# Optimization experiments

Hardware: AMD Instinct MI355X
Metric: run time of the kernel (lower is better)

The kernel has to match this reference:

```python
import jax, jax.numpy as jnp
import numpy as np
import math

B, T, D = 2, 2048, 2048
H = 16
HD = D // H
FF = D * 2


def rmsnorm(x, w):
    eps = jnp.finfo(x.dtype).eps  # torch RMSNorm default eps=None -> finfo eps
    ms = jnp.mean(jnp.square(x), axis=-1, keepdims=True)
    return x * jax.lax.rsqrt(ms + eps) * w


def setup_inputs() -> dict:
    key = jax.random.key(0)
    ks = jax.random.split(key, 8)
    s = 0.02
    return {
        "x": jax.random.normal(ks[0], (B, T, D), jnp.float32),
        "scale_gamma": jax.random.uniform(ks[1], (D,), jnp.float32, 0.5, 1.5),
        "scale_beta": jax.random.normal(ks[2], (D,), jnp.float32) * 0.1,
        "qkv_w": jax.random.normal(ks[3], (3 * D, D), jnp.float32) * s,
        "o_w": jax.random.normal(ks[4], (D, D), jnp.float32) * s,
        "gate_w": jax.random.normal(ks[5], (FF, D), jnp.float32) * s,
        "up_w": jax.random.normal(ks[6], (FF, D), jnp.float32) * s,
        "down_w": jax.random.normal(ks[7], (D, FF), jnp.float32) * s,
        "norm1_w": jnp.ones((D,), jnp.float32),
        "norm2_w": jnp.ones((D,), jnp.float32),
    }


def reference(x, scale_gamma, scale_beta, qkv_w, o_w, gate_w, up_w, down_w, norm1_w, norm2_w):
    # --- attention sub-block ---
    h = rmsnorm(x, norm1_w) * scale_gamma + scale_beta
    qkv = (h @ qkv_w.T).reshape(B, T, 3, H, HD)
    q, k, v = [jnp.transpose(qkv[:, :, i], (0, 2, 1, 3)) for i in range(3)]  # (B,H,T,HD)
    scores = jnp.einsum("bhqd,bhkd->bhqk", q, k) / math.sqrt(HD)
    causal = jnp.tril(jnp.ones((T, T), bool))
    scores = jnp.where(causal, scores, -jnp.inf)
    attn = jax.nn.softmax(scores, axis=-1)
    out = jnp.einsum("bhqk,bhkd->bhqd", attn, v)
    out = jnp.transpose(out, (0, 2, 1, 3)).reshape(B, T, D)
    x = x + out @ o_w.T
    # --- SwiGLU FFN sub-block ---
    h = rmsnorm(x, norm2_w) * scale_gamma + scale_beta
    ff = jax.nn.silu(h @ gate_w.T) * (h @ up_w.T)
    return x + ff @ down_w.T
```

## Files before the change

### kernel.cpp

```cpp
#include <hip/hip_runtime.h>
#include <cstdint>

#define D_MODEL 2048
#define T_SEQ   2048
#define BATCH   2
#define NHEAD   16
#define HDIM    128
#define FFDIM   4096
#define NTOK    4096

using bf16_t = __bf16;
typedef __attribute__((ext_vector_type(8))) __bf16 bf16x8;
typedef __attribute__((ext_vector_type(4))) __bf16 bf16x4;
typedef __attribute__((ext_vector_type(4))) float  f32x4;

typedef __attribute__((address_space(1))) void as1_void;
typedef __attribute__((address_space(3))) void as3_void;

__device__ __forceinline__ void async_copy16(const void* g, void* lds) {
  __builtin_amdgcn_global_load_lds((as1_void*)(uintptr_t)g,
                                   (as3_void*)(uint32_t)(uintptr_t)lds,
                                   16, 0, 0);
}

__device__ __forceinline__ size_t packidx(int n, int kc, int nkt) {
  int kt = kc >> 2, kg = kc & 3;
  return (((size_t)(n >> 7) * nkt + kt) << 9) + (kg << 7) + (n & 127);
}

#define NQ 1572864
#define NO 524288
#define NG 1048576
#define NU 1048576
#define ND 1048576
#define TOTC (NQ + NO + NG + NU + ND)
__global__ __launch_bounds__(256) void f2b_all_kernel(
    const float* __restrict__ s0, const float* __restrict__ s1,
    const float* __restrict__ s2, const float* __restrict__ s3,
    const float* __restrict__ s4,
    bf16_t* __restrict__ d0, bf16_t* __restrict__ d1,
    bf16_t* __restrict__ dgu, bf16_t* __restrict__ d4) {
  int c = blockIdx.x * 256 + threadIdx.x;
  const int stride = gridDim.x * 256;
  for (; c < TOTC; c += stride) {
    const float* src; bf16_t* dst; size_t didx; int sf4;
    if (c < NQ) {
      int n = c >> 8, kc = c & 255;
      src = s0; sf4 = n * 512 + kc * 2;
      dst = d0; didx = packidx(n, kc, 64);
    } else if (c < NQ + NO) {
      int lc = c - NQ, n = lc >> 8, kc = lc & 255;
      src = s1; sf4 = n * 512 + kc * 2;
      dst = d1; didx = packidx(n, kc, 64);
    } else if (c < NQ + NO + NG) {
      int lc = c - NQ - NO, g = lc >> 8, kc = lc & 255;
      int n2 = ((g >> 4) << 5) + (g & 15);
      src = s2; sf4 = g * 512 + kc * 2;
      dst = dgu; didx = packidx(n2, kc, 64);
    } else if (c < NQ + NO + NG + NU) {
      int lc = c - NQ - NO - NG, u = lc >> 8, kc = lc & 255;
      int n2 = ((u >> 4) << 5) + 16 + (u & 15);
      src = s3; sf4 = u * 512 + kc * 2;
      dst = dgu; didx = packidx(n2, kc, 64);
    } else {
      int lc = c - NQ - NO - NG - NU, n = lc >> 9, kc = lc & 511;
      src = s4; sf4 = n * 1024 + kc * 2;
      dst = d4; didx = packidx(n, kc, 128);
    }
    float4 v0 = ((const float4*)src)[sf4];
    float4 v1 = ((const float4*)src)[sf4 + 1];
    bf16x8 r;
    r[0] = (bf16_t)v0.x; r[1] = (bf16_t)v0.y; r[2] = (bf16_t)v0.z; r[3] = (bf16_t)v0.w;
    r[4] = (bf16_t)v1.x; r[5] = (bf16_t)v1.y; r[6] = (bf16_t)v1.z; r[7] = (bf16_t)v1.w;
    *(bf16x8*)(dst + didx * 8) = r;
  }
}

__global__ __launch_bounds__(256) void rmsnorm_kernel(const float* __restrict__ x,
                                                      const float* __restrict__ nw,
                                                      const float* __restrict__ gamma,
                                                      const float* __restrict__ beta,
                                                      bf16_t* __restrict__ out) {
  const int row = blockIdx.x;
  const int t = threadIdx.x;
  const float* xr = x + (size_t)row * D_MODEL;
  float4 va = ((const float4*)xr)[2 * t];
  float4 vb = ((const float4*)xr)[2 * t + 1];
  float ss = va.x*va.x + va.y*va.y + va.z*va.z + va.w*va.w
           + vb.x*vb.x + vb.y*vb.y + vb.z*vb.z + vb.w*vb.w;
#pragma unroll
  for (int off = 1; off < 64; off <<= 1) ss += __shfl_xor(ss, off, 64);
  __shared__ float sred[4];
  if ((t & 63) == 0) sred[t >> 6] = ss;
  __syncthreads();
  float tot = sred[0] + sred[1] + sred[2] + sred[3];
  float inv = rsqrtf(tot * (1.0f / D_MODEL) + 1.1920929e-07f);
  const int c0 = t * 8;
  float a8[8] = {va.x, va.y, va.z, va.w, vb.x, vb.y, vb.z, vb.w};
  bf16x8 r;
#pragma unroll
  for (int j = 0; j < 8; ++j)
    r[j] = (bf16_t)(a8[j] * inv * nw[c0 + j] * gamma[c0 + j] + beta[c0 + j]);
  *(bf16x8*)(out + packidx(row, t, 64) * 8) = r;
}

template <int EPI>
__global__ __launch_bounds__(256) void gemm_kernel(const bf16_t* __restrict__ A,
                                                   const bf16_t* __restrict__ Bw,
                                                   int M, int N, int K,
                                                   void* out, const void* aux) {
  __shared__ alignas(16) bf16_t As[2][4][128][8];
  __shared__ alignas(16) bf16_t Bs[2][4][128][8];
  const int tid = threadIdx.x;
  const int wave = tid >> 6, lane = tid & 63;
  const int quad = lane >> 4, l16 = lane & 15;
  const int bx = blockIdx.x, by = blockIdx.y;
  const int wr = (wave >> 1) * 64, wc = (wave & 1) * 64;
  const int rowA0 = by * 128, colB0 = bx * 128;

  const f32x4 fzero = {0.f, 0.f, 0.f, 0.f};
  f32x4 acc[4][4];
#pragma unroll
  for (int i = 0; i < 4; ++i)
#pragma unroll
    for (int j = 0; j < 4; ++j) acc[i][j] = fzero;

  const int nk = K >> 5;
  const bf16_t* a0 = A + ((size_t)by * nk << 12) + tid * 8;
  const bf16_t* a1 = a0 + 2048;
  const bf16_t* b0 = Bw + ((size_t)bx * nk << 12) + tid * 8;
  const bf16_t* b1 = b0 + 2048;
  char* ldsA0 = (char*)As + (wave * 64) * 16;
  char* ldsA1 = (char*)As + (256 + wave * 64) * 16;
  char* ldsB0 = (char*)Bs + (wave * 64) * 16;
  char* ldsB1 = (char*)Bs + (256 + wave * 64) * 16;

  async_copy16(a0, ldsA0);
  async_copy16(a1, ldsA1);
  async_copy16(b0, ldsB0);
  async_copy16(b1, ldsB1);
  a0 += 4096; a1 += 4096; b0 += 4096; b1 += 4096;

  for (int kt = 0; kt < nk; ++kt) {
    __syncthreads();
    const int cur = kt & 1;
    if (kt + 1 < nk) {
      const int nxt = 8192 * (1 - cur);
      async_copy16(a0, ldsA0 + nxt);
      async_copy16(a1, ldsA1 + nxt);
      async_copy16(b0, ldsB0 + nxt);
      async_copy16(b1, ldsB1 + nxt);
      a0 += 4096; a1 += 4096; b0 += 4096; b1 += 4096;
    }
    bf16x8 af[4], bfr[4];
#pragma unroll
    for (int mi = 0; mi < 4; ++mi)
      af[mi] = *(const bf16x8*)&As[cur][quad][wr + mi * 16 + l16][0];
#pragma unroll
    for (int ni = 0; ni < 4; ++ni)
      bfr[ni] = *(const bf16x8*)&Bs[cur][quad][wc + ni * 16 + l16][0];
#pragma unroll
    for (int mi = 0; mi < 4; ++mi)
#pragma unroll
      for (int ni = 0; ni < 4; ++ni)
        acc[mi][ni] = __builtin_amdgcn_mfma_f32_16x16x32_bf16(af[mi], bfr[ni],
                                                              acc[mi][ni], 0, 0, 0);
  }

  if (EPI == 4) {
#pragma unroll
    for (int mi = 0; mi < 4; ++mi) {
#pragma unroll
      for (int r = 0; r < 4; ++r) {
        const int row = rowA0 + wr + mi * 16 + quad * 4 + r;
        const int rt = row >> 7, m = row & 127;
#pragma unroll
        for (int p = 0; p < 2; ++p) {
          float g = acc[mi][2 * p][r];
          float u = acc[mi][2 * p + 1][r];
          float sv = g / (1.0f + __expf(-g));
          const int ffcol = bx * 64 + (wc >> 1) + l16 + p * 16;
          const int kt2 = ffcol >> 5, kg2 = (ffcol >> 3) & 3, e = ffcol & 7;
          const size_t idx =
              (((((size_t)rt * 128 + kt2) << 9) + (kg2 << 7) + m) << 3) + e;
          ((bf16_t*)out)[idx] = (bf16_t)(sv * u);
        }
      }
    }
  } else {
#pragma unroll
    for (int mi = 0; mi < 4; ++mi) {
#pragma unroll
      for (int r = 0; r < 4; ++r) {
        const int row = rowA0 + wr + mi * 16 + quad * 4 + r;
        const size_t base = (size_t)row * N;
#pragma unroll
        for (int ni = 0; ni < 4; ++ni) {
          const int col = colB0 + wc + ni * 16 + l16;
          const size_t idx = base + col;
          float v = acc[mi][ni][r];
          if (EPI == 0) {
            ((bf16_t*)out)[idx] = (bf16_t)v;
          } else {
            ((float*)out)[idx] = v + ((const float*)aux)[idx];
          }
        }
      }
    }
  }
}

__global__ __launch_bounds__(256) void vtrans_kernel(const bf16_t* __restrict__ qkv,
                                                     bf16_t* __restrict__ vt) {
  const int bh = blockIdx.y;
  const int b = bh >> 4, h = bh & 15;
  const int t0 = blockIdx.x << 6;
  const int tid = threadIdx.x;
  __shared__ bf16_t tile[64][136];
#pragma unroll
  for (int r = 0; r < 4; ++r) {
    int ci = r * 256 + tid;
    int t = ci >> 4, dc = ci & 15;
    bf16x8 v = *(const bf16x8*)(qkv + (size_t)(b * T_SEQ + t0 + t) * 6144 + 4096 +
                                h * HDIM + dc * 8);
    *(bf16x8*)&tile[t][dc * 8] = v;
  }
  __syncthreads();
#pragma unroll
  for (int r = 0; r < 4; ++r) {
    int ci = r * 256 + tid;
    int d = ci >> 3, ts = ci & 7;
    bf16x8 o;
#pragma unroll
    for (int j = 0; j < 8; ++j) o[j] = tile[ts * 8 + j][d];
    *(bf16x8*)(vt + ((size_t)bh * HDIM + d) * T_SEQ + t0 + ts * 8) = o;
  }
}

__global__ __launch_bounds__(256) void attn_kernel(const bf16_t* __restrict__ qkv,
                                                   const bf16_t* __restrict__ vt,
                                                   bf16_t* __restrict__ out) {
  const int bh = blockIdx.y;
  const int b = bh >> 4, h = bh & 15;
  const int qt = gridDim.x - 1 - blockIdx.x;
  const int q0 = qt << 6;
  const int tid = threadIdx.x;
  const int wave = tid >> 6, lane = tid & 63;
  const int quad = lane >> 4, l16 = lane & 15;

  __shared__ alignas(16) bf16_t Ks[2][64 * 128];
  __shared__ alignas(16) bf16_t VTs[2][128 * 64];
  __shared__ bf16_t Ps[4][16][68];

  const size_t qbase = (size_t)(b * T_SEQ + q0 + wave * 16 + l16) * 6144 + h * HDIM;
  bf16x8 qf[4];
#pragma unroll
  for (int kk = 0; kk < 4; ++kk)
    qf[kk] = *(const bf16x8*)(qkv + qbase + kk * 32 + quad * 8);

  const bf16_t* gK[4];
  const bf16_t* gV[4];
#pragma unroll
  for (int c = 0; c < 4; ++c) {
    int ci = c * 256 + tid;
    int t = ci >> 4, dcs = ci & 15;
    int dc = dcs ^ (t & 15);
    gK[c] = qkv + (size_t)(b * T_SEQ + t) * 6144 + 2048 + h * HDIM + dc * 8;
    int d = ci >> 3, tcs = ci & 7;
    int tc = tcs ^ (d & 7);
    gV[c] = vt + ((size_t)bh * HDIM + d) * T_SEQ + tc * 8;
  }
  char* ldsK = (char*)Ks + wave * 1024;
  char* ldsV = (char*)VTs + wave * 1024;

  auto stage = [&](int buf) {
#pragma unroll
    for (int c = 0; c < 4; ++c) {
      async_copy16(gK[c], ldsK + buf * 16384 + c * 4096);
      gK[c] += 64 * 6144;
    }
#pragma unroll
    for (int c = 0; c < 4; ++c) {
      async_copy16(gV[c], ldsV + buf * 16384 + c * 4096);
      gV[c] += 64;
    }
  };

  const f32x4 fzero = {0.f, 0.f, 0.f, 0.f};
  f32x4 o[8];
#pragma unroll
  for (int i = 0; i < 8; ++i) o[i] = fzero;
  float mrow[4]  = {-3.0e38f, -3.0e38f, -3.0e38f, -3.0e38f};
  float lpart[4] = {0.f, 0.f, 0.f, 0.f};

  const float sc = 0.08838834764831845f;
  const float THR = 8.0f;
  const int ktmax = qt;

  stage(0);

  for (int kt = 0; kt <= ktmax; ++kt) {
    const int cur = kt & 1;
    __syncthreads();
    if (kt < ktmax) stage(1 - cur);

    const bf16_t* Kc = &Ks[cur][0];
    const bf16_t* Vc = &VTs[cur][0];

    f32x4 s[4];
#pragma unroll
    for (int nt = 0; nt < 4; ++nt) {
      s[nt] = fzero;
#pragma unroll
      for (int kk = 0; kk < 4; ++kk) {
        int tK = nt * 16 + l16;
        int cK = kk * 4 + quad;
        bf16x8 kf = *(const bf16x8*)(Kc + (tK * 16 + (cK ^ l16)) * 8);
        s[nt] = __builtin_amdgcn_mfma_f32_16x16x32_bf16(qf[kk], kf, s[nt], 0, 0, 0);
      }
    }

    const int qr0 = q0 + wave * 16 + quad * 4;
    const bool diag = (kt == ktmax);
    float pmax[4];
#pragma unroll
    for (int r = 0; r < 4; ++r) {
      const int qr = qr0 + r;
      float mx = -3.0e38f;
#pragma unroll
      for (int nt = 0; nt < 4; ++nt) {
        float v = s[nt][r] * sc;
        if (diag) {
          int kc = kt * 64 + nt * 16 + l16;
          v = (kc <= qr) ? v : -3.0e38f;
        }
        s[nt][r] = v;
        mx = fmaxf(mx, v);
      }
      pmax[r] = mx;
    }
    bool ok = (pmax[0] <= mrow[0] + THR) & (pmax[1] <= mrow[1] + THR) &
              (pmax[2] <= mrow[2] + THR) & (pmax[3] <= mrow[3] + THR);
    if (!__all(ok)) {
      float alpha[4];
#pragma unroll
      for (int r = 0; r < 4; ++r) {
        float mx = pmax[r];
#pragma unroll
        for (int off = 1; off < 16; off <<= 1) mx = fmaxf(mx, __shfl_xor(mx, off, 16));
        float mnew = fmaxf(mrow[r], mx);
        alpha[r] = __expf(mrow[r] - mnew);
        mrow[r] = mnew;
        lpart[r] *= alpha[r];
      }
#pragma unroll
      for (int i = 0; i < 8; ++i)
#pragma unroll
        for (int r = 0; r < 4; ++r) o[i][r] *= alpha[r];
    }
#pragma unroll
    for (int r = 0; r < 4; ++r) {
#pragma unroll
      for (int nt = 0; nt < 4; ++nt) {
        float pv = __expf(s[nt][r] - mrow[r]);
        s[nt][r] = pv;
        lpart[r] += pv;
      }
    }
#pragma unroll
    for (int nt = 0; nt < 4; ++nt)
#pragma unroll
      for (int r = 0; r < 4; ++r)
        Ps[wave][quad * 4 + r][nt * 16 + l16] = (bf16_t)s[nt][r];

#pragma unroll
    for (int kk2 = 0; kk2 < 2; ++kk2) {
      const bf16_t* prow = &Ps[wave][l16][kk2 * 32 + quad * 8];
      bf16x4 p0 = *(const bf16x4*)prow;
      bf16x4 p1 = *(const bf16x4*)(prow + 4);
      bf16x8 pf;
#pragma unroll
      for (int j = 0; j < 4; ++j) { pf[j] = p0[j]; pf[4 + j] = p1[j]; }
#pragma unroll
      for (int nt2 = 0; nt2 < 8; ++nt2) {
        int dV = nt2 * 16 + l16;
        int tcV = kk2 * 4 + quad;
        bf16x8 vf = *(const bf16x8*)(Vc + (dV * 8 + (tcV ^ (dV & 7))) * 8);
        o[nt2] = __builtin_amdgcn_mfma_f32_16x16x32_bf16(pf, vf, o[nt2], 0, 0, 0);
      }
    }
  }

  float rl[4];
#pragma unroll
  for (int r = 0; r < 4; ++r) {
    float l = lpart[r];
#pragma unroll
    for (int off = 1; off < 16; off <<= 1) l += __shfl_xor(l, off, 16);
    rl[r] = 1.0f / l;
  }
#pragma unroll
  for (int nt2 = 0; nt2 < 8; ++nt2) {
#pragma unroll
    for (int r = 0; r < 4; ++r) {
      const int gt = b * T_SEQ + q0 + wave * 16 + quad * 4 + r;
      const int mt = gt >> 7, m = gt & 127;
      const int col = h * HDIM + nt2 * 16 + l16;
      const int kt2 = col >> 5, kg2 = (col >> 3) & 3, e = col & 7;
      const size_t idx = (((((size_t)mt * 64 + kt2) << 9) + (kg2 << 7) + m) << 3) + e;
      out[idx] = (bf16_t)(o[nt2][r] * rl[r]);
    }
  }
}

extern "C" void kernel_launch(void* const* d_in, const int* in_sizes, int n_in,
                              void* d_out, int out_size, void* d_ws, size_t ws_size,
                              hipStream_t stream) {
  const float* x      = (const float*)d_in[0];
  const float* gamma  = (const float*)d_in[1];
  const float* beta   = (const float*)d_in[2];
  const float* qkv_w  = (const float*)d_in[3];
  const float* o_w    = (const float*)d_in[4];
  const float* gate_w = (const float*)d_in[5];
  const float* up_w   = (const float*)d_in[6];
  const float* down_w = (const float*)d_in[7];
  const float* n1w    = (const float*)d_in[8];
  const float* n2w    = (const float*)d_in[9];
  float* out = (float*)d_out;

  char* p = (char*)d_ws;
  bf16_t* qkv_wb  = (bf16_t*)p; p += (size_t)3 * D_MODEL * D_MODEL * 2;
  bf16_t* o_wb    = (bf16_t*)p; p += (size_t)D_MODEL * D_MODEL * 2;
  bf16_t* gu_wb   = (bf16_t*)p; p += (size_t)2 * FFDIM * D_MODEL * 2;
  bf16_t* down_wb = (bf16_t*)p; p += (size_t)D_MODEL * FFDIM * 2;
  bf16_t* h_b     = (bf16_t*)p; p += (size_t)NTOK * D_MODEL * 2;
  bf16_t* qkv_b   = (bf16_t*)p; p += (size_t)NTOK * 3 * D_MODEL * 2;
  bf16_t* attn_b  = (bf16_t*)p; p += (size_t)NTOK * D_MODEL * 2;
  float*  x1      = (float*)p;  p += (size_t)NTOK * D_MODEL * 4;
  bf16_t* g_b     = (bf16_t*)p; p += (size_t)NTOK * FFDIM * 2;
  bf16_t* vt_b    = g_b;

  dim3 blk(256);
  f2b_all_kernel<<<dim3(2048), blk, 0, stream>>>(
      qkv_w, o_w, gate_w, up_w, down_w,
      qkv_wb, o_wb, gu_wb, down_wb);

  rmsnorm_kernel<<<dim3(NTOK), blk, 0, stream>>>(x, n1w, gamma, beta, h_b);
  gemm_kernel<0><<<dim3(3 * D_MODEL / 128, NTOK / 128), blk, 0, stream>>>(
      h_b, qkv_wb, NTOK, 3 * D_MODEL, D_MODEL, qkv_b, nullptr);
  vtrans_kernel<<<dim3(T_SEQ / 64, BATCH * NHEAD), blk, 0, stream>>>(qkv_b, vt_b);
  attn_kernel<<<dim3(T_SEQ / 64, BATCH * NHEAD), blk, 0, stream>>>(qkv_b, vt_b, attn_b);
  gemm_kernel<1><<<dim3(D_MODEL / 128, NTOK / 128), blk, 0, stream>>>(
      attn_b, o_wb, NTOK, D_MODEL, D_MODEL, x1, x);

  rmsnorm_kernel<<<dim3(NTOK), blk, 0, stream>>>(x1, n2w, gamma, beta, h_b);
  gemm_kernel<4><<<dim3(2 * FFDIM / 128, NTOK / 128), blk, 0, stream>>>(
      h_b, gu_wb, NTOK, 2 * FFDIM, D_MODEL, g_b, nullptr);
  gemm_kernel<1><<<dim3(D_MODEL / 128, NTOK / 128), blk, 0, stream>>>(
      g_b, down_wb, NTOK, D_MODEL, FFDIM, out, x1);
}
```

Baseline: 815.3 us.

## Add 256x256-tile GEMM with 4-stage async pipeline for QKV and gate/up

Introduces a 512-thread GEMM kernel with 256x256 output tiles, a 4-deep LDS ring of async global-to-LDS copies, interleaved load/MFMA phases with priority hints, and an XCD-aware block swizzle. It replaces the 128x128 GEMM for the QKV projection and the fused gate/up SwiGLU GEMM, aiming at more data reuse per tile and better overlap of loads with compute. The old kernel's SwiGLU epilogue is removed. Tradeoffs are 128KB of LDS, higher register pressure and fewer blocks on these grids.

```diff
diff --git a/kernel.cpp b/kernel.cpp
--- a/kernel.cpp
+++ b/kernel.cpp
@@ -21,6 +21,10 @@
   __builtin_amdgcn_global_load_lds((as1_void*)(uintptr_t)g,
                                    (as3_void*)(uint32_t)(uintptr_t)lds,
                                    16, 0, 0);
+}
+
+__device__ __forceinline__ void barrier_raw() {
+  asm volatile("s_barrier" ::: "memory");
 }
 
 __device__ __forceinline__ size_t packidx(int n, int kc, int nkt) {
@@ -105,6 +109,133 @@
 }
 
 template <int EPI>
+__global__ __launch_bounds__(512, 2) void gemm256_kernel(
+    const bf16_t* __restrict__ A, const bf16_t* __restrict__ Bw,
+    int M, int N, int K, void* out) {
+  __shared__ alignas(16) char ldsbuf[131072];
+  const int tid = threadIdx.x;
+  const int wave = tid >> 6, lane = tid & 63;
+  const int quad = lane >> 4, l16 = lane & 15;
+  const int wm = wave >> 2, wn = wave & 3;
+
+  const int gx = gridDim.x;
+  const int lin = blockIdx.y * gx + blockIdx.x;
+  const int cpx = (gx * gridDim.y) >> 3;
+  const int swz = (lin & 7) * cpx + (lin >> 3);
+  const int bx = swz % gx, by = swz / gx;
+
+  const int nk = K >> 5;
+  const char* pA0 = (const char*)A  + (((size_t)(2 * by)     * nk) << 13) + tid * 16;
+  const char* pA1 = (const char*)A  + (((size_t)(2 * by + 1) * nk) << 13) + tid * 16;
+  const char* pB0 = (const char*)Bw + (((size_t)(2 * bx)     * nk) << 13) + tid * 16;
+  const char* pB1 = (const char*)Bw + (((size_t)(2 * bx + 1) * nk) << 13) + tid * 16;
+
+  auto stageA = [&](int b) {
+    async_copy16(pA0, ldsbuf + (b << 15) + wave * 1024);
+    async_copy16(pA1, ldsbuf + (b << 15) + 8192 + wave * 1024);
+    pA0 += 8192; pA1 += 8192;
+  };
+  auto stageB = [&](int b) {
+    async_copy16(pB0, ldsbuf + (b << 15) + 16384 + wave * 1024);
+    async_copy16(pB1, ldsbuf + (b << 15) + 24576 + wave * 1024);
+    pB0 += 8192; pB1 += 8192;
+  };
+
+  const f32x4 fzero = {0.f, 0.f, 0.f, 0.f};
+  f32x4 acc[8][4];
+#pragma unroll
+  for (int i = 0; i < 8; ++i)
+#pragma unroll
+    for (int j = 0; j < 4; ++j) acc[i][j] = fzero;
+
+  stageA(0); stageB(0); stageA(1); stageB(1); stageA(2); stageB(2);
+  asm volatile("s_waitcnt vmcnt(8)" ::: "memory");
+  barrier_raw();
+
+  for (int j = 0; j < nk; ++j) {
+    const int b = j & 3;
+    const int bs = (b + 3) & 3;
+    const bool more = (j + 3 < nk);
+    const char* Ab = ldsbuf + (b << 15) + (wm << 13) + (quad << 11);
+    const char* Bb = ldsbuf + (b << 15) + 16384 + ((wn >> 1) << 13) + (quad << 11) +
+                     ((wn & 1) << 10);
+    bf16x8 af[4], bfr[4];
+#pragma unroll
+    for (int mi = 0; mi < 4; ++mi)
+      af[mi] = *(const bf16x8*)(Ab + (mi * 16 + l16) * 16);
+#pragma unroll
+    for (int ni = 0; ni < 4; ++ni)
+      bfr[ni] = *(const bf16x8*)(Bb + (ni * 16 + l16) * 16);
+    if (more) stageA(bs);
+    barrier_raw();
+    __builtin_amdgcn_s_setprio(1);
+#pragma unroll
+    for (int mi = 0; mi < 4; ++mi)
+#pragma unroll
+      for (int ni = 0; ni < 4; ++ni)
+        acc[mi][ni] = __builtin_amdgcn_mfma_f32_16x16x32_bf16(af[mi], bfr[ni],
+                                                              acc[mi][ni], 0, 0, 0);
+    __builtin_amdgcn_s_setprio(0);
+    barrier_raw();
+#pragma unroll
+    for (int mi = 0; mi < 4; ++mi)
+      af[mi] = *(const bf16x8*)(Ab + ((mi + 4) * 16 + l16) * 16);
+    if (more) stageB(bs);
+    barrier_raw();
+    __builtin_amdgcn_s_setprio(1);
+#pragma unroll
+    for (int mi = 0; mi < 4; ++mi)
+#pragma unroll
+      for (int ni = 0; ni < 4; ++ni)
+        acc[mi + 4][ni] = __builtin_amdgcn_mfma_f32_16x16x32_bf16(af[mi], bfr[ni],
+                                                                  acc[mi + 4][ni], 0, 0, 0);
+    __builtin_amdgcn_s_setprio(0);
+    if (j + 3 < nk)      asm volatile("s_waitcnt vmcnt(8)" ::: "memory");
+    else if (j + 2 < nk) asm volatile("s_waitcnt vmcnt(4)" ::: "memory");
+    else if (j + 1 < nk) asm volatile("s_waitcnt vmcnt(0)" ::: "memory");
+    barrier_raw();
+  }
+
+  const int rowbase = by * 256 + wm * 128;
+  const int colbase = bx * 256 + wn * 64;
+  if (EPI == 4) {
+#pragma unroll
+    for (int mi = 0; mi < 8; ++mi) {
+#pragma unroll
+      for (int r = 0; r < 4; ++r) {
+        const int row = rowbase + mi * 16 + quad * 4 + r;
+        const int rt = row >> 7, m = row & 127;
+#pragma unroll
+        for (int p = 0; p < 2; ++p) {
+          float g = acc[mi][2 * p][r];
+          float u = acc[mi][2 * p + 1][r];
+          float sv = g / (1.0f + __expf(-g));
+          const int ffcol = (bx * 8 + wn * 2 + p) * 16 + l16;
+          const int kt2 = ffcol >> 5, kg2 = (ffcol >> 3) & 3, e = ffcol & 7;
+          const size_t idx =
+              (((((size_t)rt * 128 + kt2) << 9) + (kg2 << 7) + m) << 3) + e;
+          ((bf16_t*)out)[idx] = (bf16_t)(sv * u);
+        }
+      }
+    }
+  } else {
+#pragma unroll
+    for (int mi = 0; mi < 8; ++mi) {
+#pragma unroll
+      for (int r = 0; r < 4; ++r) {
+        const int row = rowbase + mi * 16 + quad * 4 + r;
+        const size_t base = (size_t)row * N;
+#pragma unroll
+        for (int ni = 0; ni < 4; ++ni) {
+          const int col = colbase + ni * 16 + l16;
+          ((bf16_t*)out)[base + col] = (bf16_t)acc[mi][ni][r];
+        }
+      }
+    }
+  }
+}
+
+template <int EPI>
 __global__ __launch_bounds__(256) void gemm_kernel(const bf16_t* __restrict__ A,
                                                    const bf16_t* __restrict__ Bw,
                                                    int M, int N, int K,
@@ -167,43 +298,21 @@
                                                               acc[mi][ni], 0, 0, 0);
   }
 
-  if (EPI == 4) {
-#pragma unroll
-    for (int mi = 0; mi < 4; ++mi) {
-#pragma unroll
-      for (int r = 0; r < 4; ++r) {
-        const int row = rowA0 + wr + mi * 16 + quad * 4 + r;
-        const int rt = row >> 7, m = row & 127;
-#pragma unroll
-        for (int p = 0; p < 2; ++p) {
-          float g = acc[mi][2 * p][r];
-          float u = acc[mi][2 * p + 1][r];
-          float sv = g / (1.0f + __expf(-g));
-          const int ffcol = bx * 64 + (wc >> 1) + l16 + p * 16;
-          const int kt2 = ffcol >> 5, kg2 = (ffcol >> 3) & 3, e = ffcol & 7;
-          const size_t idx =
-              (((((size_t)rt * 128 + kt2) << 9) + (kg2 << 7) + m) << 3) + e;
-          ((bf16_t*)out)[idx] = (bf16_t)(sv * u);
-        }
-      }
-    }
-  } else {
-#pragma unroll
-    for (int mi = 0; mi < 4; ++mi) {
-#pragma unroll
-      for (int r = 0; r < 4; ++r) {
-        const int row = rowA0 + wr + mi * 16 + quad * 4 + r;
-        const size_t base = (size_t)row * N;
-#pragma unroll
-        for (int ni = 0; ni < 4; ++ni) {
-          const int col = colB0 + wc + ni * 16 + l16;
-          const size_t idx = base + col;
-          float v = acc[mi][ni][r];
-          if (EPI == 0) {
-            ((bf16_t*)out)[idx] = (bf16_t)v;
-          } else {
-            ((float*)out)[idx] = v + ((const float*)aux)[idx];
-          }
+#pragma unroll
+  for (int mi = 0; mi < 4; ++mi) {
+#pragma unroll
+    for (int r = 0; r < 4; ++r) {
+      const int row = rowA0 + wr + mi * 16 + quad * 4 + r;
+      const size_t base = (size_t)row * N;
+#pragma unroll
+      for (int ni = 0; ni < 4; ++ni) {
+        const int col = colB0 + wc + ni * 16 + l16;
+        const size_t idx = base + col;
+        float v = acc[mi][ni][r];
+        if (EPI == 0) {
+          ((bf16_t*)out)[idx] = (bf16_t)v;
+        } else {
+          ((float*)out)[idx] = v + ((const float*)aux)[idx];
         }
       }
     }
@@ -441,21 +550,22 @@
   bf16_t* vt_b    = g_b;
 
   dim3 blk(256);
+  dim3 blk512(512);
   f2b_all_kernel<<<dim3(2048), blk, 0, stream>>>(
       qkv_w, o_w, gate_w, up_w, down_w,
       qkv_wb, o_wb, gu_wb, down_wb);
 
   rmsnorm_kernel<<<dim3(NTOK), blk, 0, stream>>>(x, n1w, gamma, beta, h_b);
-  gemm_kernel<0><<<dim3(3 * D_MODEL / 128, NTOK / 128), blk, 0, stream>>>(
-      h_b, qkv_wb, NTOK, 3 * D_MODEL, D_MODEL, qkv_b, nullptr);
+  gemm256_kernel<0><<<dim3(3 * D_MODEL / 256, NTOK / 256), blk512, 0, stream>>>(
+      h_b, qkv_wb, NTOK, 3 * D_MODEL, D_MODEL, qkv_b);
   vtrans_kernel<<<dim3(T_SEQ / 64, BATCH * NHEAD), blk, 0, stream>>>(qkv_b, vt_b);
   attn_kernel<<<dim3(T_SEQ / 64, BATCH * NHEAD), blk, 0, stream>>>(qkv_b, vt_b, attn_b);
   gemm_kernel<1><<<dim3(D_MODEL / 128, NTOK / 128), blk, 0, stream>>>(
       attn_b, o_wb, NTOK, D_MODEL, D_MODEL, x1, x);
 
   rmsnorm_kernel<<<dim3(NTOK), blk, 0, stream>>>(x1, n2w, gamma, beta, h_b);
-  gemm_kernel<4><<<dim3(2 * FFDIM / 128, NTOK / 128), blk, 0, stream>>>(
-      h_b, gu_wb, NTOK, 2 * FFDIM, D_MODEL, g_b, nullptr);
+  gemm256_kernel<4><<<dim3(2 * FFDIM / 256, NTOK / 256), blk512, 0, stream>>>(
+      h_b, gu_wb, NTOK, 2 * FFDIM, D_MODEL, g_b);
   gemm_kernel<1><<<dim3(D_MODEL / 128, NTOK / 128), blk, 0, stream>>>(
       g_b, down_wb, NTOK, D_MODEL, FFDIM, out, x1);
 }
```

Result: slower. 833.4 us (+2.2%).
